# Optimization experiments

Hardware: AMD Instinct MI355X
Metric: run time of the kernel (lower is better)

Reference implementation:

```python
import jax, jax.numpy as jnp
import numpy as np

FEATURE_DIM = 1024
HEADS = 16
HEAD_DIM = FEATURE_DIM // HEADS


def setup_inputs() -> dict:
    key = jax.random.key(0)
    ks = jax.random.split(key, 9)
    B, C, T = 4, FEATURE_DIM, 4096
    s = 1.0 / np.sqrt(C)
    inp = {
        "x": jax.random.normal(ks[0], (B, C, T), dtype=jnp.float32),
        "Wq": jax.random.uniform(ks[1], (C, C), jnp.float32, -s, s),
        "bq": jax.random.uniform(ks[2], (C,), jnp.float32, -s, s),
        "Wk": jax.random.uniform(ks[3], (C, C), jnp.float32, -s, s),
        "bk": jax.random.uniform(ks[4], (C,), jnp.float32, -s, s),
        "Wv": jax.random.uniform(ks[5], (C, C), jnp.float32, -s, s),
        "bv": jax.random.uniform(ks[6], (C,), jnp.float32, -s, s),
        "Wo": jax.random.uniform(ks[7], (C, C), jnp.float32, -s, s),
        "bo": jax.random.uniform(ks[8], (C,), jnp.float32, -s, s),
    }
    return inp


def reference(x, Wq, bq, Wk, bk, Wv, bv, Wo, bo):
    B, C, T = x.shape
    H, D = HEADS, HEAD_DIM
    xt = jnp.transpose(x, (0, 2, 1))  # [B, T, C]
    # torch Linear: y = x @ W.T + b
    q = jax.nn.elu(xt @ Wq.T + bq).reshape(B, T, H, D) + 1.0
    k = jax.nn.elu(xt @ Wk.T + bk).reshape(B, T, H, D) + 1.0
    v = (xt @ Wv.T + bv).reshape(B, T, H, D)
    kv = jnp.einsum('bthd,bthe->bhde', k, v)      # [B, H, D, D]
    z = jnp.einsum('bthd,bhd->bth', q, k.sum(axis=1))  # [B, T, H]
    num = jnp.einsum('bthd,bhde->bthe', q, kv)    # [B, T, H, D]
    out = num / (z[..., None] + 1e-6)
    out = out.reshape(B, T, C)
    out = out @ Wo.T + bo  # dropout is identity in eval mode
    return jnp.transpose(out + xt, (0, 2, 1))  # [B, C, T]
```

## Files before the change

### kernel.cpp

```cpp
#include <hip/hip_runtime.h>
#include <hip/hip_bf16.h>
#include <cmath>

typedef unsigned short u16;
typedef unsigned int   u32;

#define BB 4
#define CC 1024
#define TT 4096
#define HH 16
#define DD 64

using bf16x8 = __attribute__((ext_vector_type(8))) __bf16;
using f32x4  = __attribute__((ext_vector_type(4))) float;

union FragU { bf16x8 v; u16 u[8]; };

__device__ __forceinline__ float bf2f(u16 u) {
    union { u32 i; float f; } v; v.i = ((u32)u) << 16; return v.f;
}
__device__ __forceinline__ u16 f2bf(float f) {
    union { float f; u32 i; } v; v.f = f;
    u32 x = v.i;
    return (u16)((x + 0x7fffu + ((x >> 16) & 1u)) >> 16);
}

__device__ __forceinline__ void gl_lds16(const u16* g, u16* l) {
    __builtin_amdgcn_global_load_lds(
        (const __attribute__((address_space(1))) void*)g,
        (__attribute__((address_space(3))) void*)l, 16, 0, 0);
}

__global__ __launch_bounds__(256) void prep_kernel(
    const float* __restrict__ x,
    const float* __restrict__ Wq, const float* __restrict__ Wk,
    const float* __restrict__ Wv, const float* __restrict__ Wo,
    u16* __restrict__ xt, u16* __restrict__ Wcat, u16* __restrict__ Wob,
    float* __restrict__ kvz)
{
    __shared__ u16 tile[64 * 258];
    const int id  = blockIdx.x;
    const int tid = threadIdx.x;

    if (id < 1024) {
        const int t0 = (id & 63) * 64;
        const int c0 = ((id >> 6) & 3) * 256;
        const int b  = id >> 8;
        const float* xb  = x  + (size_t)b * CC * TT;
        u16*         xtb = xt + (size_t)b * TT * CC;
        const int tcol = tid & 63;
        const int rw   = tid >> 6;
        #pragma unroll 8
        for (int p = 0; p < 64; ++p) {
            const int cr = p * 4 + rw;
            tile[tcol * 258 + cr] = f2bf(xb[(size_t)(c0 + cr) * TT + t0 + tcol]);
        }
        __syncthreads();
        const int cp = tid & 127;
        const int th = tid >> 7;
        #pragma unroll 8
        for (int q = 0; q < 32; ++q) {
            const int tr = q * 2 + th;
            const u32 v = *reinterpret_cast<const u32*>(&tile[tr * 258 + cp * 2]);
            *reinterpret_cast<u32*>(&xtb[(size_t)(t0 + tr) * CC + c0 + cp * 2]) = v;
        }
    } else if (id < 5120) {
        const int id2  = id - 1024;
        const int wsel = id2 >> 10;
        const int i    = ((id2 & 1023) * 256 + tid) * 4;
        const float* src = (wsel == 0) ? Wq : (wsel == 1) ? Wk : (wsel == 2) ? Wv : Wo;
        u16* dst = (wsel < 3) ? (Wcat + (size_t)wsel * CC * CC) : Wob;
        const float4 v = *reinterpret_cast<const float4*>(src + i);
        ushort4 o;
        o.x = f2bf(v.x); o.y = f2bf(v.y); o.z = f2bf(v.z); o.w = f2bf(v.w);
        *reinterpret_cast<ushort4*>(dst + i) = o;
    } else {
        const int idx = ((id - 5120) * 256 + tid) * 4;
        *reinterpret_cast<float4*>(&kvz[idx]) = (float4){0.f, 0.f, 0.f, 0.f};
    }
}

__device__ __forceinline__ bf16x8 ldfrag(const u16* Xs, int row, int kk, int quad, int l7) {
    return *reinterpret_cast<const bf16x8*>(&Xs[row * 64 + ((((kk << 2) | quad) ^ l7) << 3)]);
}

__global__ __launch_bounds__(512, 2) void qkv_kernel(
    const u16* __restrict__ A, const u16* __restrict__ W,
    const float* __restrict__ bq, const float* __restrict__ bk,
    const float* __restrict__ bv, u16* __restrict__ Ybf)
{
    __shared__ __align__(16) u16 As[2][256 * 64];
    __shared__ __align__(16) u16 Bs[2][256 * 64];

    const int tid  = threadIdx.x;
    const int w    = tid >> 6;
    const int lane = tid & 63;
    const int wm   = w >> 2;
    const int wn   = w & 3;
    const int quad = lane >> 4;
    const int l16  = lane & 15;
    const int l7   = l16 & 7;

    const int bid = blockIdx.x;
    const int wg  = (bid & 7) * 96 + (bid >> 3);
    const int m0  = (wg / 12) * 256;
    const int n0  = (wg % 12) * 256;

    const u16* Ag = A + (size_t)m0 * CC;
    const u16* Wg = W + (size_t)n0 * CC;

    const int r8 = lane >> 3;
    const int cg = ((lane & 7) ^ r8) * 8;

#define STG(Xg, Xs, h, kt)                                                          \
    { _Pragma("unroll")                                                             \
      for (int s_ = 0; s_ < 2; ++s_)                                                \
        gl_lds16((Xg) + (size_t)((h) * 128 + w * 16 + s_ * 8 + r8) * CC             \
                     + (kt) * 64 + cg,                                              \
                 &(Xs)[((h) * 128 + w * 16 + s_ * 8) * 64]); }

#define BAR() { asm volatile("" ::: "memory"); __builtin_amdgcn_s_barrier(); \
                asm volatile("" ::: "memory"); }
#define LGKM0() asm volatile("s_waitcnt lgkmcnt(0)" ::: "memory")

    STG(Ag, As[0], 0, 0);
    STG(Wg, Bs[0], 1, 0);
    STG(Ag, As[0], 1, 0);
    STG(Wg, Bs[0], 0, 0);
    STG(Ag, As[1], 0, 1);
    STG(Wg, Bs[1], 1, 1);
    STG(Ag, As[1], 1, 1);
    asm volatile("s_waitcnt vmcnt(6)" ::: "memory");
    BAR();

    f32x4 acc[8][4];
    #pragma unroll
    for (int i = 0; i < 8; ++i)
        #pragma unroll
        for (int jj = 0; jj < 4; ++jj) acc[i][jj] = (f32x4)0.0f;

    bf16x8 af[4][2];
    bf16x8 bf[2][2];

#define LOAD_A(MH, CUR)                                                             \
    { _Pragma("unroll")                                                             \
      for (int i_ = 0; i_ < 4; ++i_)                                                \
        _Pragma("unroll")                                                           \
        for (int kk_ = 0; kk_ < 2; ++kk_)                                           \
          af[i_][kk_] = ldfrag(&As[CUR][0],                                         \
              wm * 128 + (MH) * 64 + i_ * 16 + l16, kk_, quad, l7); }

#define LOAD_B(NH, CUR)                                                             \
    { _Pragma("unroll")                                                             \
      for (int jl_ = 0; jl_ < 2; ++jl_)                                             \
        _Pragma("unroll")                                                           \
        for (int kk_ = 0; kk_ < 2; ++kk_)                                           \
          bf[jl_][kk_] = ldfrag(&Bs[CUR][0],                                        \
              wn * 64 + (NH) * 32 + jl_ * 16 + l16, kk_, quad, l7); }

#define MFMA_Q(MH, NH)                                                              \
    { __builtin_amdgcn_s_setprio(1);                                                \
      _Pragma("unroll")                                                             \
      for (int kk_ = 0; kk_ < 2; ++kk_)                                             \
        _Pragma("unroll")                                                           \
        for (int i_ = 0; i_ < 4; ++i_)                                              \
          _Pragma("unroll")                                                         \
          for (int jl_ = 0; jl_ < 2; ++jl_)                                         \
            acc[(MH) * 4 + i_][(NH) * 2 + jl_] =                                    \
              __builtin_amdgcn_mfma_f32_16x16x32_bf16(af[i_][kk_],                  \
                  bf[jl_][kk_], acc[(MH) * 4 + i_][(NH) * 2 + jl_], 0, 0, 0);       \
      __builtin_amdgcn_s_setprio(0); }

#define BLOCK(CUR, NXT, J, S0, S123, VM)                                            \
  {                                                                                 \
                                   \
    LOAD_A(0, CUR); LOAD_B(0, CUR);                                                 \
    if (S0)   { STG(Wg, Bs[NXT], 0, (J) + 1); }                                     \
    BAR(); LGKM0();                                                                 \
    MFMA_Q(0, 0);                                                                   \
    BAR();                                                                          \
                                           \
    LOAD_B(1, CUR);                                                                 \
    if (S123) { STG(Ag, As[CUR], 0, (J) + 2); }                                     \
    BAR(); LGKM0();                                                                 \
    MFMA_Q(0, 1);                                                                   \
    BAR();                                                                          \
                                           \
    LOAD_A(1, CUR);                                                                 \
    if (S123) { STG(Wg, Bs[CUR], 1, (J) + 2); }                                     \
    BAR(); LGKM0();                                                                 \
    MFMA_Q(1, 1);                                                                   \
    BAR();                                                                          \
                    \
    LOAD_B(0, CUR);                                                                 \
    if (S123) { STG(Ag, As[CUR], 1, (J) + 2); }                                     \
    BAR(); LGKM0();                                                                 \
    MFMA_Q(1, 0);                                                                   \
    if ((VM) == 6)      { asm volatile("s_waitcnt vmcnt(6)" ::: "memory"); }        \
    else if ((VM) == 0) { asm volatile("s_waitcnt vmcnt(0)" ::: "memory"); }        \
    BAR();                                                                          \
  }

    for (int j = 0; j < 14; j += 2) {
        BLOCK(0, 1, j,     1, 1, 6);
        BLOCK(1, 0, j + 1, 1, 1, 6);
    }
    BLOCK(0, 1, 14, 1, 0, 0);
    BLOCK(1, 0, 15, 0, 0, -1);

#undef BLOCK
#undef MFMA_Q
#undef LOAD_B
#undef LOAD_A
#undef LGKM0
#undef BAR
#undef STG

    const int seg = n0 >> 10;
    const int nL  = n0 & 1023;
    if (seg == 0) {
        #pragma unroll
        for (int i = 0; i < 8; ++i) {
            const int row = m0 + wm * 128 + i * 16 + quad * 4;
            #pragma unroll
            for (int jj = 0; jj < 4; ++jj) {
                const int col = nL + wn * 64 + jj * 16 + l16;
                const float bvs = bq[col];
                #pragma unroll
                for (int r = 0; r < 4; ++r) {
                    float v = acc[i][jj][r] + bvs;
                    v = (v > 0.0f) ? (v + 1.0f) : __expf(v);
                    Ybf[(size_t)(row + r) * CC + col] = f2bf(v);
                }
            }
        }
    } else {
        const float* bp = (seg == 1) ? bk : bv;
        u16* Yt = Ybf + (size_t)seg * (size_t)(BB * TT) * CC;
        const int b  = m0 / TT;
        const int tb = m0 - b * TT + wm * 128;
        #pragma unroll
        for (int i = 0; i < 8; ++i) {
            const int t = tb + i * 16 + quad * 4;
            #pragma unroll
            for (int jj = 0; jj < 4; ++jj) {
                const int col = nL + wn * 64 + jj * 16 + l16;
                const float bvs = bp[col];
                ushort4 o;
                #pragma unroll
                for (int r = 0; r < 4; ++r) {
                    float v = acc[i][jj][r] + bvs;
                    if (seg == 1) v = (v > 0.0f) ? (v + 1.0f) : __expf(v);
                    ((u16*)&o)[r] = f2bf(v);
                }
                *reinterpret_cast<ushort4*>(
                    &Yt[((size_t)(b * CC + col)) * TT + t]) = o;
            }
        }
    }
}

template <int MODE>
__global__ __launch_bounds__(256, 2) void gemm_kernel(
    const u16* __restrict__ A, const u16* __restrict__ W,
    const float* __restrict__ b0, const float* __restrict__ b1,
    const float* __restrict__ b2, u16* __restrict__ Ybf,
    float* __restrict__ Yf, const float* __restrict__ xres,
    int M, int N, int K)
{
    __shared__ char smem[34048];
    u16* As = (u16*)smem;
    u16* Ws = (u16*)(smem + 16384);

    const int tid  = threadIdx.x;
    const int w    = tid >> 6;
    const int lane = tid & 63;
    const int wm = w >> 1, wn = w & 1;
    const int quad = lane >> 4, l16 = lane & 15;
    const int m0 = blockIdx.y * 128;
    const int n0 = blockIdx.x * 128;

    const int srow = lane >> 3;
    const int scol = ((lane & 7) ^ srow) * 8;

    f32x4 acc[4][4];
    #pragma unroll
    for (int i = 0; i < 4; ++i)
        #pragma unroll
        for (int j = 0; j < 4; ++j) acc[i][j] = (f32x4)0.0f;

    for (int k0 = 0; k0 < K; k0 += 64) {
        __syncthreads();
        #pragma unroll
        for (int s = 0; s < 4; ++s)
            gl_lds16(A + (size_t)(m0 + 32 * w + 8 * s + srow) * K + k0 + scol,
                     &As[(32 * w + 8 * s) * 64]);
        #pragma unroll
        for (int s = 0; s < 4; ++s)
            gl_lds16(W + (size_t)(n0 + 32 * w + 8 * s + srow) * K + k0 + scol,
                     &Ws[(32 * w + 8 * s) * 64]);
        __syncthreads();

        #pragma unroll
        for (int sub = 0; sub < 2; ++sub) {
            const int pg = (((sub << 2) | quad) ^ (l16 & 7)) * 8;
            bf16x8 af[4], bfr[4];
            #pragma unroll
            for (int i = 0; i < 4; ++i) {
                af[i]  = *reinterpret_cast<const bf16x8*>(&As[(wm * 64 + i * 16 + l16) * 64 + pg]);
                bfr[i] = *reinterpret_cast<const bf16x8*>(&Ws[(wn * 64 + i * 16 + l16) * 64 + pg]);
            }
            #pragma unroll
            for (int i = 0; i < 4; ++i)
                #pragma unroll
                for (int j = 0; j < 4; ++j)
                    acc[i][j] = __builtin_amdgcn_mfma_f32_16x16x32_bf16(af[i], bfr[j], acc[i][j], 0, 0, 0);
        }
    }

    if (MODE == 2) {
        float* Cs = (float*)smem;
        const int b     = m0 / TT;
        const int tbase = m0 - b * TT;
        const int cl    = lane >> 4;
        #pragma unroll
        for (int hh = 0; hh < 2; ++hh) {
            __syncthreads();
            if (wm == hh) {
                #pragma unroll
                for (int i = 0; i < 4; ++i)
                    #pragma unroll
                    for (int j = 0; j < 4; ++j)
                        #pragma unroll
                        for (int r = 0; r < 4; ++r)
                            Cs[(i * 16 + quad * 4 + r) * 133 + wn * 64 + j * 16 + l16] = acc[i][j][r];
            }
            __syncthreads();
            #pragma unroll
            for (int p = 0; p < 8; ++p) {
                const int col = p * 16 + w * 4 + cl;
                const int tl  = l16 * 4;
                float4 v;
                v.x = Cs[(tl + 0) * 133 + col];
                v.y = Cs[(tl + 1) * 133 + col];
                v.z = Cs[(tl + 2) * 133 + col];
                v.w = Cs[(tl + 3) * 133 + col];
                const float bv = b0[n0 + col];
                const size_t base = ((size_t)b * CC + n0 + col) * TT + tbase + hh * 64 + tl;
                const float4 rx = *reinterpret_cast<const float4*>(&xres[base]);
                v.x += bv + rx.x; v.y += bv + rx.y;
                v.z += bv + rx.z; v.w += bv + rx.w;
                *reinterpret_cast<float4*>(&Yf[base]) = v;
            }
        }
    }
}

__global__ __launch_bounds__(256) void kv_kernel(
    const u16* __restrict__ Kt, const u16* __restrict__ Vt,
    float* __restrict__ kv, float* __restrict__ ksum)
{
    __shared__ u16 Ks[64 * 64];
    __shared__ u16 Vs[64 * 64];
    const int bh = blockIdx.x;
    const int b = bh >> 4, h = bh & 15;
    const int tc0 = blockIdx.y * 512;
    const int tid = threadIdx.x;
    const int w = tid >> 6, lane = tid & 63;
    const int quad = lane >> 4, l16 = lane & 15;

    const u16* Kg = Kt + ((size_t)(b * CC + h * DD)) * TT;
    const u16* Vg = Vt + ((size_t)(b * CC + h * DD)) * TT;

    const int srow = lane >> 3;
    const int scol = ((lane & 7) ^ srow) * 8;

    f32x4 acc[4];
    #pragma unroll
    for (int j = 0; j < 4; ++j) acc[j] = (f32x4)0.0f;
    f32x4 ks = (f32x4)0.0f;

    FragU ones;
    #pragma unroll
    for (int j = 0; j < 8; ++j) ones.u[j] = (l16 == 0) ? 0x3F80u : 0u;

    for (int it = 0; it < 8; ++it) {
        const int t0 = tc0 + it * 64;
        __syncthreads();
        #pragma unroll
        for (int s = 0; s < 2; ++s) {
            gl_lds16(Kg + (size_t)(16 * w + 8 * s + srow) * TT + t0 + scol,
                     &Ks[(16 * w + 8 * s) * 64]);
            gl_lds16(Vg + (size_t)(16 * w + 8 * s + srow) * TT + t0 + scol,
                     &Vs[(16 * w + 8 * s) * 64]);
        }
        __syncthreads();

        #pragma unroll
        for (int sub = 0; sub < 2; ++sub) {
            const int pg = (((sub << 2) | quad) ^ (l16 & 7)) * 8;
            const bf16x8 af = *reinterpret_cast<const bf16x8*>(
                &Ks[(w * 16 + l16) * 64 + pg]);
            #pragma unroll
            for (int e4 = 0; e4 < 4; ++e4) {
                const bf16x8 bfv = *reinterpret_cast<const bf16x8*>(
                    &Vs[(e4 * 16 + l16) * 64 + pg]);
                acc[e4] = __builtin_amdgcn_mfma_f32_16x16x32_bf16(af, bfv, acc[e4], 0, 0, 0);
            }
            ks = __builtin_amdgcn_mfma_f32_16x16x32_bf16(af, ones.v, ks, 0, 0, 0);
        }
    }

    float* kvb = kv + (size_t)bh * DD * DD;
    #pragma unroll
    for (int e4 = 0; e4 < 4; ++e4)
        #pragma unroll
        for (int r = 0; r < 4; ++r)
            atomicAdd(&kvb[(w * 16 + quad * 4 + r) * DD + e4 * 16 + l16], acc[e4][r]);
    if (l16 == 0) {
        #pragma unroll
        for (int r = 0; r < 4; ++r)
            atomicAdd(&ksum[bh * DD + w * 16 + quad * 4 + r], ks[r]);
    }
}

__global__ __launch_bounds__(256) void attn_kernel(
    const u16* __restrict__ Q, const float* __restrict__ kv,
    const float* __restrict__ ksum, u16* __restrict__ attn)
{
    __shared__ u16 Qs[256 * 64];
    __shared__ float kvs[DD * DD];
    __shared__ float kss[DD];
    const int bh = blockIdx.x;
    const int b = bh >> 4, h = bh & 15;
    const int tb = blockIdx.y * 256;
    const int tid = threadIdx.x;
    const int w = tid >> 6, lane = tid & 63;
    const int quad = lane >> 4, l16 = lane & 15;

    {
        const int srow = lane >> 3;
        const int scol = ((lane & 7) ^ srow) * 8;
        const u16* Qg = Q + ((size_t)(b * TT + tb)) * CC + h * DD;
        #pragma unroll
        for (int p = 0; p < 8; ++p)
            gl_lds16(Qg + (size_t)(64 * w + 8 * p + srow) * CC + scol,
                     &Qs[(64 * w + 8 * p) * 64]);
    }
    {
        const float4* s4 = reinterpret_cast<const float4*>(kv + (size_t)bh * DD * DD);
        float4* d4 = reinterpret_cast<float4*>(kvs);
        #pragma unroll
        for (int p = 0; p < 4; ++p) d4[p * 256 + tid] = s4[p * 256 + tid];
        if (tid < DD) kss[tid] = ksum[bh * DD + tid];
    }
    __syncthreads();

    FragU bf[4][2], zb[2];
    #pragma unroll
    for (int ck = 0; ck < 2; ++ck) {
        #pragma unroll
        for (int nt = 0; nt < 4; ++nt)
            #pragma unroll
            for (int j = 0; j < 8; ++j)
                bf[nt][ck].u[j] = f2bf(kvs[(ck * 32 + quad * 8 + j) * DD + nt * 16 + l16]);
        #pragma unroll
        for (int j = 0; j < 8; ++j)
            zb[ck].u[j] = (l16 == 0) ? f2bf(kss[ck * 32 + quad * 8 + j]) : 0u;
    }

    f32x4 acc[4][4], zacc[4];
    #pragma unroll
    for (int i = 0; i < 4; ++i) {
        zacc[i] = (f32x4)0.0f;
        #pragma unroll
        for (int j = 0; j < 4; ++j) acc[i][j] = (f32x4)0.0f;
    }

    #pragma unroll
    for (int i = 0; i < 4; ++i) {
        const int trow = w * 64 + i * 16 + l16;
        #pragma unroll
        for (int ck = 0; ck < 2; ++ck) {
            const int pg = (((ck << 2) | quad) ^ (l16 & 7)) * 8;
            const bf16x8 af = *reinterpret_cast<const bf16x8*>(&Qs[trow * 64 + pg]);
            #pragma unroll
            for (int nt = 0; nt < 4; ++nt)
                acc[i][nt] = __builtin_amdgcn_mfma_f32_16x16x32_bf16(af, bf[nt][ck].v, acc[i][nt], 0, 0, 0);
            zacc[i] = __builtin_amdgcn_mfma_f32_16x16x32_bf16(af, zb[ck].v, zacc[i], 0, 0, 0);
        }
    }

    u16* obase = attn + ((size_t)b * TT) * CC + h * DD;
    #pragma unroll
    for (int i = 0; i < 4; ++i) {
        float inv[4];
        #pragma unroll
        for (int r = 0; r < 4; ++r) {
            const float zv = __shfl(zacc[i][r], lane & 48);
            inv[r] = 1.0f / (zv + 1e-6f);
        }
        #pragma unroll
        for (int nt = 0; nt < 4; ++nt) {
            #pragma unroll
            for (int r = 0; r < 4; ++r) {
                const int t = tb + w * 64 + i * 16 + quad * 4 + r;
                obase[(size_t)t * CC + nt * 16 + l16] = f2bf(acc[i][nt][r] * inv[r]);
            }
        }
    }
}

extern "C" void kernel_launch(void* const* d_in, const int* in_sizes, int n_in,
                              void* d_out, int out_size, void* d_ws, size_t ws_size,
                              hipStream_t stream)
{
    const float* x  = (const float*)d_in[0];
    const float* Wq = (const float*)d_in[1];
    const float* bq = (const float*)d_in[2];
    const float* Wk = (const float*)d_in[3];
    const float* bk = (const float*)d_in[4];
    const float* Wv = (const float*)d_in[5];
    const float* bv = (const float*)d_in[6];
    const float* Wo = (const float*)d_in[7];
    const float* bo = (const float*)d_in[8];
    float* out = (float*)d_out;

    const int M = BB * TT;
    const size_t BUF  = (size_t)BB * TT * CC * sizeof(u16);
    const size_t WBUF = (size_t)CC * CC * sizeof(u16);

    char* ws = (char*)d_ws;
    u16* xt   = (u16*)(ws);
    u16* Qb   = (u16*)(ws + BUF);
    u16* Wcat = (u16*)(ws + 4 * BUF);
    u16* Wob  = (u16*)(ws + 4 * BUF + 3 * WBUF);
    float* kvbuf = (float*)(ws + 4 * BUF + 4 * WBUF);
    float* ksumb = kvbuf + (size_t)BB * HH * DD * DD;
    u16* attn = xt;

    prep_kernel<<<5380, 256, 0, stream>>>(x, Wq, Wk, Wv, Wo, xt, Wcat, Wob, kvbuf);

    qkv_kernel<<<768, 512, 0, stream>>>(xt, Wcat, bq, bk, bv, Qb);

    kv_kernel<<<dim3(BB * HH, TT / 512), 256, 0, stream>>>(
        Qb + (size_t)M * CC, Qb + 2 * (size_t)M * CC, kvbuf, ksumb);

    attn_kernel<<<dim3(BB * HH, TT / 256), 256, 0, stream>>>(Qb, kvbuf, ksumb, attn);

    gemm_kernel<2><<<dim3(CC / 128, M / 128), 256, 0, stream>>>(
        attn, Wob, bo, nullptr, nullptr, nullptr, out, x, M, CC, CC);
}
```

Baseline: 362.5 us.

## Prefetch next LDS fragments during MFMA and halve barriers in QKV GEMM loop

```diff
diff --git a/kernel.cpp b/kernel.cpp
--- a/kernel.cpp
+++ b/kernel.cpp
@@ -139,15 +139,16 @@
         #pragma unroll
         for (int jj = 0; jj < 4; ++jj) acc[i][jj] = (f32x4)0.0f;
 
-    bf16x8 af[4][2];
+    bf16x8 af0[4][2];
+    bf16x8 af1[4][2];
     bf16x8 bf[2][2];
 
-#define LOAD_A(MH, CUR)                                                             \
+#define LOAD_AF(AF, MH, CUR)                                                        \
     { _Pragma("unroll")                                                             \
       for (int i_ = 0; i_ < 4; ++i_)                                                \
         _Pragma("unroll")                                                           \
         for (int kk_ = 0; kk_ < 2; ++kk_)                                           \
-          af[i_][kk_] = ldfrag(&As[CUR][0],                                         \
+          AF[i_][kk_] = ldfrag(&As[CUR][0],                                         \
               wm * 128 + (MH) * 64 + i_ * 16 + l16, kk_, quad, l7); }
 
 #define LOAD_B(NH, CUR)                                                             \
@@ -158,7 +159,7 @@
           bf[jl_][kk_] = ldfrag(&Bs[CUR][0],                                        \
               wn * 64 + (NH) * 32 + jl_ * 16 + l16, kk_, quad, l7); }
 
-#define MFMA_Q(MH, NH)                                                              \
+#define MFMA_Q(AF, MH, NH)                                                          \
     { __builtin_amdgcn_s_setprio(1);                                                \
       _Pragma("unroll")                                                             \
       for (int kk_ = 0; kk_ < 2; ++kk_)                                             \
@@ -167,43 +168,44 @@
           _Pragma("unroll")                                                         \
           for (int jl_ = 0; jl_ < 2; ++jl_)                                         \
             acc[(MH) * 4 + i_][(NH) * 2 + jl_] =                                    \
-              __builtin_amdgcn_mfma_f32_16x16x32_bf16(af[i_][kk_],                  \
+              __builtin_amdgcn_mfma_f32_16x16x32_bf16(AF[i_][kk_],                  \
                   bf[jl_][kk_], acc[(MH) * 4 + i_][(NH) * 2 + jl_], 0, 0, 0);       \
       __builtin_amdgcn_s_setprio(0); }
 
-#define BLOCK(CUR, NXT, J, S0, S123, VM)                                            \
+#define BLOCK(CUR, NXT, J, S0, S123, VM3)                                           \
   {                                                                                 \
-                                   \
-    LOAD_A(0, CUR); LOAD_B(0, CUR);                                                 \
+          \
+          \
+    LOAD_AF(af0, 0, CUR); LOAD_B(0, CUR);                                           \
     if (S0)   { STG(Wg, Bs[NXT], 0, (J) + 1); }                                     \
-    BAR(); LGKM0();                                                                 \
-    MFMA_Q(0, 0);                                                                   \
+    LGKM0();                                                                        \
+    MFMA_Q(af0, 0, 0);                                                              \
+    LOAD_B(1, CUR);                                                                 \
     BAR();                                                                          \
-                                           \
-    LOAD_B(1, CUR);                                                                 \
+                               \
+    LGKM0();                                                                        \
     if (S123) { STG(Ag, As[CUR], 0, (J) + 2); }                                     \
-    BAR(); LGKM0();                                                                 \
-    MFMA_Q(0, 1);                                                                   \
+    MFMA_Q(af0, 0, 1);                                                              \
+    LOAD_AF(af1, 1, CUR);                                                           \
     BAR();                                                                          \
-                                           \
-    LOAD_A(1, CUR);                                                                 \
+                       \
+    LGKM0();                                                                        \
     if (S123) { STG(Wg, Bs[CUR], 1, (J) + 2); }                                     \
-    BAR(); LGKM0();                                                                 \
-    MFMA_Q(1, 1);                                                                   \
+    MFMA_Q(af1, 1, 1);                                                              \
+    LOAD_B(0, CUR);                                                                 \
     BAR();                                                                          \
-                    \
-    LOAD_B(0, CUR);                                                                 \
+                 \
+    if ((VM3) == 4)      { asm volatile("s_waitcnt vmcnt(4)" ::: "memory"); }       \
+    else if ((VM3) == 0) { asm volatile("s_waitcnt vmcnt(0)" ::: "memory"); }       \
+    LGKM0();                                                                        \
     if (S123) { STG(Ag, As[CUR], 1, (J) + 2); }                                     \
-    BAR(); LGKM0();                                                                 \
-    MFMA_Q(1, 0);                                                                   \
-    if ((VM) == 6)      { asm volatile("s_waitcnt vmcnt(6)" ::: "memory"); }        \
-    else if ((VM) == 0) { asm volatile("s_waitcnt vmcnt(0)" ::: "memory"); }        \
+    MFMA_Q(af1, 1, 0);                                                              \
     BAR();                                                                          \
   }
 
     for (int j = 0; j < 14; j += 2) {
-        BLOCK(0, 1, j,     1, 1, 6);
-        BLOCK(1, 0, j + 1, 1, 1, 6);
+        BLOCK(0, 1, j,     1, 1, 4);
+        BLOCK(1, 0, j + 1, 1, 1, 4);
     }
     BLOCK(0, 1, 14, 1, 0, 0);
     BLOCK(1, 0, 15, 0, 0, -1);
@@ -211,7 +213,7 @@
 #undef BLOCK
 #undef MFMA_Q
 #undef LOAD_B
-#undef LOAD_A
+#undef LOAD_AF
 #undef LGKM0
 #undef BAR
 #undef STG
```

Result: faster. 355.2 us (-2.0%).
